# Performance work log

Measured on AMD Instinct MI355X. Metric: run time of the kernel, lower is better.

The kernel has to match this reference:

```python
import jax, jax.numpy as jnp
import numpy as np

B, N = 4, 512
NF, EF = 12, 1          # node / edge feature dims (fixed in GraphClassifier)
QK = 128                # baseFeatNum -> QKDims = nValDims
NV_D, EV_D = 128, 32    # nValDims, eValDims
TR = 2 * NV_D           # Trans output = nValDims*2 = 256
NCLS = 5
EPS = 1e-5


def setup_inputs() -> dict:
    key = jax.random.key(0)
    ks = jax.random.split(key, 16)
    s = 0.1
    return {
        "nodes": jax.random.normal(ks[0], (B, N, NF), jnp.float32),
        "edges": jax.random.normal(ks[1], (B, N, N, EF), jnp.float32),
        "distances": jax.random.uniform(ks[2], (B, N, N), jnp.float32),
        "mask": jax.random.randint(ks[3], (B, N, N), 0, 2) > 0,
        "Wq": jax.random.normal(ks[4], (QK, NF), jnp.float32) * s,
        "bq": jnp.zeros((QK,), jnp.float32),
        "Wk": jax.random.normal(ks[5], (QK, NF), jnp.float32) * s,
        "bk": jnp.zeros((QK,), jnp.float32),
        "Wnv": jax.random.normal(ks[6], (NV_D, NF), jnp.float32) * s,
        "bnv": jnp.zeros((NV_D,), jnp.float32),
        "Wev": jax.random.normal(ks[7], (EV_D, EF), jnp.float32) * s,
        "bev": jnp.zeros((EV_D,), jnp.float32),
        "Wt": jax.random.normal(ks[8], (TR, NV_D + EV_D), jnp.float32) * s,
        "bt": jnp.zeros((TR,), jnp.float32),
        "gamma": jnp.ones((TR,), jnp.float32),
        "beta": jnp.zeros((TR,), jnp.float32),
        "Wc": jax.random.normal(ks[9], (NCLS, TR), jnp.float32) * s,
        "bc": jnp.zeros((NCLS,), jnp.float32),
    }


def reference(nodes, edges, distances, mask, Wq, bq, Wk, bk, Wnv, bnv,
              Wev, bev, Wt, bt, gamma, beta, Wc, bc):
    coeff = 1.0 / np.sqrt(QK).astype(np.float32)
    Q = nodes @ Wq.T + bq            # (b,N,QK)
    K = nodes @ Wk.T + bk            # (b,N,QK)
    NV = nodes @ Wnv.T + bnv         # (b,N,nValDims); NV[b,i,j]=NV_node[b,j] after repeat
    EV = edges @ Wev.T + bev         # (b,N,N,eValDims)

    dist_w = 1.0 / (distances + 1.0)
    scores = jnp.einsum('bik,bjk->bij', Q, K) * dist_w * coeff
    scores = jnp.where(mask, -jnp.inf, scores)
    w = jax.nn.softmax(scores, axis=-1)
    w = jnp.where(jnp.isnan(w), 0.0, w)  # fully-masked rows -> zero weights

    node_part = jnp.einsum('bij,bjd->bid', w, NV)     # weighted node values
    edge_part = jnp.einsum('bij,bijd->bid', w, EV)    # weighted edge values
    vals = jnp.concatenate([node_part, edge_part], axis=-1)
    vals = jnp.tanh(vals) @ Wt.T + bt                 # (b,N,2*nValDims)

    # BatchNorm1d in training mode: biased batch stats over (b*N)
    flat = vals.reshape(-1, TR)
    mu = flat.mean(axis=0)
    var = flat.var(axis=0)
    flat = (flat - mu) / jnp.sqrt(var + EPS) * gamma + beta
    vals = flat.reshape(vals.shape)

    return vals @ Wc.T + bc                           # (b,N,5)
```

## Files before the change

kernel.cpp:

```cpp
#include <hip/hip_runtime.h>
#include <math.h>

#define NNODE 512
#define NBATCH 4
#define NFEAT 12
#define QKD 128
#define NVD 128
#define EVD 32
#define CATD 160
#define CATB 168
#define TRD 256
#define NCLS 5
#define NROWS 2048
#define EPSV 1e-5f
#define NSTATBUF 8
#define NCHUNK 4
#define JC 128
#define RPB 8
#define SSW 132
#define WBW 136

typedef float floatx4 __attribute__((ext_vector_type(4)));
typedef __bf16 bf16x8 __attribute__((ext_vector_type(8)));
typedef unsigned short ushort_t;
typedef ushort_t ushort4v __attribute__((ext_vector_type(4)));

static __device__ __forceinline__ ushort_t f2bf(float x) {
  unsigned int u = __float_as_uint(x);
  return (ushort_t)((u + 0x7fffu + ((u >> 16) & 1u)) >> 16);
}
static __device__ __forceinline__ int slot32(int r) {
  return ((r & 15) >> 2) * 8 + (r & 3) + ((r >> 4) << 2);
}
static __device__ __forceinline__ int kslot(int k) {
  return (k & ~31) + slot32(k & 31);
}

__global__ __launch_bounds__(256) void qkv_kernel(
    const float* __restrict__ nodes,
    const float* __restrict__ Wq, const float* __restrict__ bq,
    const float* __restrict__ Wk, const float* __restrict__ bk,
    const float* __restrict__ Wnv, const float* __restrict__ bnv,
    const float* __restrict__ Wt,
    ushort_t* __restrict__ Qb, ushort_t* __restrict__ Kb,
    ushort_t* __restrict__ NVT, ushort_t* __restrict__ Wtb,
    float* __restrict__ stats) {
  const int tid = threadIdx.x;
  const int blk = blockIdx.x;
  const int rowbase = blk * 8;
  const int b = rowbase >> 9;
  const int jloc = rowbase & (NNODE - 1);
  if (blk < 2 * NSTATBUF) stats[blk * 256 + tid] = 0.f;
  if (tid < CATD)
    Wtb[(size_t)blk * CATD + kslot(tid)] = f2bf(Wt[(size_t)blk * CATD + tid]);
  __shared__ float sn[RPB][NFEAT];
  if (tid < RPB * NFEAT) ((float*)sn)[tid] = nodes[(size_t)rowbase * NFEAT + tid];
  __syncthreads();

  {
    const int d  = tid & 127;
    const int rg = tid >> 7;
    const int sd = kslot(d);
    float wq[NFEAT], wk[NFEAT];
#pragma unroll
    for (int k = 0; k < NFEAT; ++k) {
      wq[k] = Wq[d * NFEAT + k];
      wk[k] = Wk[d * NFEAT + k];
    }
    const float bqv = bq[d], bkv = bk[d];
#pragma unroll
    for (int rr = 0; rr < 4; ++rr) {
      const int rl = rg * 4 + rr;
      float aq = bqv, ak = bkv;
#pragma unroll
      for (int k = 0; k < NFEAT; ++k) {
        const float n = sn[rl][k];
        aq = fmaf(n, wq[k], aq);
        ak = fmaf(n, wk[k], ak);
      }
      Qb[(size_t)(rowbase + rl) * QKD + sd] = f2bf(aq);
      Kb[(size_t)(rowbase + rl) * QKD + sd] = f2bf(ak);
    }
  }
  {
    const int d    = tid >> 1;
    const int half = tid & 1;
    float wnv[NFEAT];
#pragma unroll
    for (int k = 0; k < NFEAT; ++k) wnv[k] = Wnv[d * NFEAT + k];
    const float bnvv = bnv[d];
    ushort4v v;
#pragma unroll
    for (int e = 0; e < 4; ++e) {
      const int rl = half * 4 + e;
      float av = bnvv;
#pragma unroll
      for (int k = 0; k < NFEAT; ++k) av = fmaf(sn[rl][k], wnv[k], av);
      v[e] = f2bf(av);
    }
    const int js = jloc + half * 4;
    const int jsl = (js & ~31) + slot32(js & 31);
    *(ushort4v*)(NVT + (size_t)b * QKD * NNODE + (size_t)d * NNODE + jsl) = v;
  }
}

__global__ __launch_bounds__(512) void attnTrans_kernel(
    const ushort_t* __restrict__ Qb, const ushort_t* __restrict__ Kb,
    const ushort_t* __restrict__ NVT,
    const float* __restrict__ edges, const float* __restrict__ dist,
    const int* __restrict__ mask,
    const float* __restrict__ Wev, const float* __restrict__ bev,
    const ushort_t* __restrict__ Wtb, const float* __restrict__ bt,
    float* __restrict__ vals, float* __restrict__ stats) {
  __shared__ __align__(16) float sS[2][RPB][SSW];
  __shared__ __align__(16) ushort_t sWb[2][16][WBW];
  __shared__ __align__(16) ushort_t catb[RPB * CATB];
  __shared__ float sF[16], sF2[RPB], sSe[RPB], sSw[RPB];

  const int tid = threadIdx.x;
  const int bid = blockIdx.x;
  const int b   = bid >> 6;
  const int rg  = bid & 63;
  const int rowbase = b * NNODE + rg * RPB;

  const int lane = tid & 63;
  const int wv   = tid >> 6;
  const int col  = lane & 15;
  const int kg   = lane >> 4;

  if (tid < 16) sF[tid] = 0.f;

  const int jl  = wv * 16 + col;
  const int dpv = wv * 16 + col;

  bf16x8 aq[4];
  {
    const ushort_t* Qr = Qb + (size_t)(rowbase + (col & 7)) * QKD;
#pragma unroll
    for (int ks = 0; ks < 4; ++ks)
      aq[ks] = *(const bf16x8*)(Qr + ks * 32 + kg * 8);
  }

  bf16x8 kf[2][4], nf[2][4];
  float dd[2][4]; int mm[2][4];
  float ee0[2], ee1[2];
  {
    const ushort_t* Kr = Kb + (size_t)(b * NNODE + jl) * QKD;
    const ushort_t* Nr = NVT + ((size_t)b * QKD + dpv) * NNODE;
#pragma unroll
    for (int ks = 0; ks < 4; ++ks) {
      kf[0][ks] = *(const bf16x8*)(Kr + ks * 32 + kg * 8);
      nf[0][ks] = *(const bf16x8*)(Nr + ks * 32 + kg * 8);
    }
#pragma unroll
    for (int r = 0; r < 4; ++r) {
      const size_t off = (size_t)(rowbase + ((kg * 4 + r) & 7)) * NNODE + jl;
      dd[0][r] = dist[off];
      mm[0][r] = mask[off];
    }
    ee0[0] = edges[(size_t)(rowbase + wv) * NNODE + lane];
    ee1[0] = edges[(size_t)(rowbase + wv) * NNODE + 64 + lane];
  }

  float m_run = -__builtin_inff(), l_run = 0.f, se_run = 0.f;
  floatx4 acc = {0.f, 0.f, 0.f, 0.f};
  const float coeff = 0.0883883476483184f;

#pragma unroll
  for (int c = 0; c < NCHUNK; ++c) {
    const int cur = c & 1, nxt = (c + 1) & 1;
    if (c + 1 < NCHUNK) {
      const int jb2 = (c + 1) * JC;
      const ushort_t* Kr = Kb + (size_t)(b * NNODE + jb2 + jl) * QKD;
      const ushort_t* Nr = NVT + ((size_t)b * QKD + dpv) * NNODE + jb2;
#pragma unroll
      for (int ks = 0; ks < 4; ++ks) {
        kf[nxt][ks] = *(const bf16x8*)(Kr + ks * 32 + kg * 8);
        nf[nxt][ks] = *(const bf16x8*)(Nr + ks * 32 + kg * 8);
      }
#pragma unroll
      for (int r = 0; r < 4; ++r) {
        const size_t off =
            (size_t)(rowbase + ((kg * 4 + r) & 7)) * NNODE + jb2 + jl;
        dd[nxt][r] = dist[off];
        mm[nxt][r] = mask[off];
      }
      ee0[nxt] = edges[(size_t)(rowbase + wv) * NNODE + jb2 + lane];
      ee1[nxt] = edges[(size_t)(rowbase + wv) * NNODE + jb2 + 64 + lane];
    }

    {
      floatx4 sc = {0.f, 0.f, 0.f, 0.f};
#pragma unroll
      for (int ks = 0; ks < 4; ++ks)
        sc = __builtin_amdgcn_mfma_f32_16x16x32_bf16(aq[ks], kf[cur][ks], sc,
                                                     0, 0, 0);
      if (kg < 2) {
#pragma unroll
        for (int r = 0; r < 4; ++r) {
          float s = sc[r] * coeff / (dd[cur][r] + 1.0f);
          if (mm[cur][r]) s = -__builtin_inff();
          sS[cur][kg * 4 + r][jl] = s;
        }
      }
    }
    __syncthreads();

    {
      const float v0 = sS[cur][wv][lane];
      const float v1 = sS[cur][wv][lane + 64];
      float mc = fmaxf(v0, v1);
#pragma unroll
      for (int s = 1; s < 64; s <<= 1) mc = fmaxf(mc, __shfl_xor(mc, s, 64));
      const float mn = fmaxf(m_run, mc);
      const float f = (m_run > -__builtin_inff()) ? __expf(m_run - mn) : 0.f;
      float w0 = 0.f, w1 = 0.f;
      if (mn > -__builtin_inff()) {
        w0 = __expf(v0 - mn);
        w1 = __expf(v1 - mn);
      }
      const int j0 = lane, j1 = lane + 64;
      sWb[cur][wv][(j0 & ~31) + slot32(j0 & 31)] = f2bf(w0);
      sWb[cur][wv][(j1 & ~31) + slot32(j1 & 31)] = f2bf(w1);
      float lc = w0 + w1;
      float sec = fmaf(w0, ee0[cur], w1 * ee1[cur]);
#pragma unroll
      for (int s = 1; s < 64; s <<= 1) {
        lc  += __shfl_xor(lc, s, 64);
        sec += __shfl_xor(sec, s, 64);
      }
      l_run  = l_run * f + lc;
      se_run = se_run * f + sec;
      m_run  = mn;
      if (lane == 0) sF[wv] = f;
    }
    __syncthreads();

    {
      acc[0] *= sF[kg * 4 + 0];
      acc[1] *= sF[kg * 4 + 1];
      acc[2] *= sF[kg * 4 + 2];
      acc[3] *= sF[kg * 4 + 3];
#pragma unroll
      for (int ks = 0; ks < 4; ++ks) {
        const bf16x8 aw =
            *(const bf16x8*)(&sWb[cur][col][ks * 32 + kg * 8]);
        acc = __builtin_amdgcn_mfma_f32_16x16x32_bf16(aw, nf[cur][ks], acc,
                                                      0, 0, 0);
      }
    }
  }

  {
    const float inv = (l_run > 0.f) ? 1.f / l_run : 0.f;
    if (lane == 0) {
      sF2[wv] = inv;
      sSe[wv] = se_run * inv;
      sSw[wv] = (l_run > 0.f) ? 1.f : 0.f;
    }
  }
  __syncthreads();

  if (kg < 2) {
#pragma unroll
    for (int r = 0; r < 4; ++r) {
      const int row = kg * 4 + r;
      catb[row * CATB + kslot(dpv)] = f2bf(tanhf(acc[r] * sF2[row]));
    }
  }
  if (tid < RPB * EVD) {
    const int r = tid >> 5, de = tid & 31;
    catb[r * CATB + 128 + slot32(de)] =
        f2bf(tanhf(fmaf(Wev[de], sSe[r], bev[de] * sSw[r])));
  }
  __syncthreads();

  {
    bf16x8 af[5];
    const ushort_t* cr = catb + (size_t)(col & 7) * CATB;
#pragma unroll
    for (int ks = 0; ks < 5; ++ks)
      af[ks] = *(const bf16x8*)(cr + ks * 32 + kg * 8);
    float* sbuf = stats + (size_t)(bid & (NSTATBUF - 1)) * 2 * TRD;
#pragma unroll
    for (int t = 0; t < 2; ++t) {
      const int o = (wv * 2 + t) * 16 + col;
      const ushort_t* wr = Wtb + (size_t)o * CATD;
      floatx4 a2 = {0.f, 0.f, 0.f, 0.f};
#pragma unroll
      for (int ks = 0; ks < 5; ++ks) {
        const bf16x8 bf = *(const bf16x8*)(wr + ks * 32 + kg * 8);
        a2 = __builtin_amdgcn_mfma_f32_16x16x32_bf16(af[ks], bf, a2, 0, 0, 0);
      }
      const float bto = bt[o];
      float s1 = 0.f, s2 = 0.f;
#pragma unroll
      for (int r = 0; r < 4; ++r) {
        const float v2 = a2[r] + bto;
        if (kg < 2) {
          vals[(size_t)(rowbase + kg * 4 + r) * TRD + o] = v2;
          s1 += v2;
          s2 = fmaf(v2, v2, s2);
        }
      }
      s1 += __shfl_xor(s1, 16, 64); s2 += __shfl_xor(s2, 16, 64);
      s1 += __shfl_xor(s1, 32, 64); s2 += __shfl_xor(s2, 32, 64);
      if (kg == 0) {
        atomicAdd(&sbuf[o], s1);
        atomicAdd(&sbuf[TRD + o], s2);
      }
    }
  }
}

__global__ __launch_bounds__(256) void outbn_kernel(
    const float* __restrict__ vals, const float* __restrict__ stats,
    const float* __restrict__ gamma, const float* __restrict__ beta,
    const float* __restrict__ Wc, const float* __restrict__ bc,
    float* __restrict__ out) {
  __shared__ float sW[NCLS][TRD];
  __shared__ float sb[NCLS];
  __shared__ float red[4][NCLS];
  const int tid = threadIdx.x;
  const int o = tid;
  float s1 = 0.f, s2 = 0.f;
#pragma unroll
  for (int k = 0; k < NSTATBUF; ++k) {
    s1 += stats[k * 2 * TRD + o];
    s2 += stats[k * 2 * TRD + TRD + o];
  }
  const float invN = 1.0f / (float)NROWS;
  const float mu  = s1 * invN;
  const float var = s2 * invN - mu * mu;
  const float inv = 1.0f / sqrtf(var + EPSV);
  const float g = gamma[o] * inv;
  const float bterm = beta[o] - mu * g;
  float v[NCLS];
#pragma unroll
  for (int c = 0; c < NCLS; ++c) {
    const float wc = Wc[c * TRD + o];
    sW[c][o] = wc * g;
    v[c] = wc * bterm;
  }
#pragma unroll
  for (int s = 1; s < 64; s <<= 1) {
#pragma unroll
    for (int c = 0; c < NCLS; ++c) v[c] += __shfl_xor(v[c], s, 64);
  }
  if ((tid & 63) == 0) {
#pragma unroll
    for (int c = 0; c < NCLS; ++c) red[tid >> 6][c] = v[c];
  }
  __syncthreads();
  if (tid < NCLS)
    sb[tid] = bc[tid] + red[0][tid] + red[1][tid] + red[2][tid] + red[3][tid];
  __syncthreads();

  const int lane = tid & 63;
  const int row = blockIdx.x * 4 + (tid >> 6);
  float vv[TRD / 64];
#pragma unroll
  for (int t = 0; t < TRD / 64; ++t)
    vv[t] = vals[(size_t)row * TRD + lane + 64 * t];
#pragma unroll
  for (int c = 0; c < NCLS; ++c) {
    float p = 0.f;
#pragma unroll
    for (int t = 0; t < TRD / 64; ++t)
      p = fmaf(vv[t], sW[c][lane + 64 * t], p);
#pragma unroll
    for (int s = 1; s < 64; s <<= 1) p += __shfl_xor(p, s, 64);
    if (lane == 0) out[(size_t)row * NCLS + c] = p + sb[c];
  }
}

extern "C" void kernel_launch(void* const* d_in, const int* in_sizes, int n_in,
                              void* d_out, int out_size, void* d_ws, size_t ws_size,
                              hipStream_t stream) {
  (void)in_sizes; (void)n_in; (void)out_size; (void)ws_size;
  const float* nodes = (const float*)d_in[0];
  const float* edges = (const float*)d_in[1];
  const float* dist  = (const float*)d_in[2];
  const int*   mask  = (const int*)d_in[3];
  const float* Wq  = (const float*)d_in[4];
  const float* bq  = (const float*)d_in[5];
  const float* Wk  = (const float*)d_in[6];
  const float* bk  = (const float*)d_in[7];
  const float* Wnv = (const float*)d_in[8];
  const float* bnv = (const float*)d_in[9];
  const float* Wev = (const float*)d_in[10];
  const float* bev = (const float*)d_in[11];
  const float* Wt  = (const float*)d_in[12];
  const float* bt  = (const float*)d_in[13];
  const float* gamma = (const float*)d_in[14];
  const float* beta  = (const float*)d_in[15];
  const float* Wc  = (const float*)d_in[16];
  const float* bc  = (const float*)d_in[17];

  char* w = (char*)d_ws;
  ushort_t* Qb  = (ushort_t*)w;                w += (size_t)NROWS * QKD * 2;
  ushort_t* Kb  = (ushort_t*)w;                w += (size_t)NROWS * QKD * 2;
  ushort_t* NVT = (ushort_t*)w;                w += (size_t)NBATCH * QKD * NNODE * 2;
  ushort_t* Wtb = (ushort_t*)w;                w += (size_t)TRD * CATD * 2;
  float* vals  = (float*)w;                    w += (size_t)NROWS * TRD * 4;
  float* stats = (float*)w;
  float* outp  = (float*)d_out;

  qkv_kernel<<<NROWS / RPB, 256, 0, stream>>>(nodes, Wq, bq, Wk, bk, Wnv, bnv,
                                              Wt, Qb, Kb, NVT, Wtb, stats);
  attnTrans_kernel<<<NROWS / RPB, 512, 0, stream>>>(
      Qb, Kb, NVT, edges, dist, mask, Wev, bev, Wtb, bt, vals, stats);
  outbn_kernel<<<NROWS / 4, 256, 0, stream>>>(vals, stats, gamma, beta,
                                              Wc, bc, outp);
}
```

Baseline: 31.91 us.

## Halve rows per attention block, use 4 waves each owning two column tiles

The attention+Trans kernel now handles 4 query rows per block with 256 threads instead of 8 rows with 512, doubling the grid to 512 blocks. Each wave computes two 16-column score and value tiles, and the Trans GEMM loops over four output tiles per wave. This is meant to raise block count and occupancy across CUs and cut per-block sync cost. In exchange, K/NV fragments are loaded by twice as many blocks and 3/4 of MFMA rows are wasted since only 4 of 16 rows are valid.

```diff
diff --git a/kernel.cpp b/kernel.cpp
--- a/kernel.cpp
+++ b/kernel.cpp
@@ -16,7 +16,8 @@
 #define NSTATBUF 8
 #define NCHUNK 4
 #define JC 128
-#define RPB 8
+#define RPB 4
+#define QR 8
 #define SSW 132
 #define WBW 136
 
@@ -47,14 +48,14 @@
     float* __restrict__ stats) {
   const int tid = threadIdx.x;
   const int blk = blockIdx.x;
-  const int rowbase = blk * 8;
+  const int rowbase = blk * QR;
   const int b = rowbase >> 9;
   const int jloc = rowbase & (NNODE - 1);
   if (blk < 2 * NSTATBUF) stats[blk * 256 + tid] = 0.f;
   if (tid < CATD)
     Wtb[(size_t)blk * CATD + kslot(tid)] = f2bf(Wt[(size_t)blk * CATD + tid]);
-  __shared__ float sn[RPB][NFEAT];
-  if (tid < RPB * NFEAT) ((float*)sn)[tid] = nodes[(size_t)rowbase * NFEAT + tid];
+  __shared__ float sn[QR][NFEAT];
+  if (tid < QR * NFEAT) ((float*)sn)[tid] = nodes[(size_t)rowbase * NFEAT + tid];
   __syncthreads();
 
   {
@@ -104,7 +105,7 @@
   }
 }
 
-__global__ __launch_bounds__(512) void attnTrans_kernel(
+__global__ __launch_bounds__(256) void attnTrans_kernel(
     const ushort_t* __restrict__ Qb, const ushort_t* __restrict__ Kb,
     const ushort_t* __restrict__ NVT,
     const float* __restrict__ edges, const float* __restrict__ dist,
@@ -119,8 +120,8 @@
 
   const int tid = threadIdx.x;
   const int bid = blockIdx.x;
-  const int b   = bid >> 6;
-  const int rg  = bid & 63;
+  const int b   = bid >> 7;
+  const int rg  = bid & 127;
   const int rowbase = b * NNODE + rg * RPB;
 
   const int lane = tid & 63;
@@ -130,40 +131,56 @@
 
   if (tid < 16) sF[tid] = 0.f;
 
-  const int jl  = wv * 16 + col;
-  const int dpv = wv * 16 + col;
+  const int jl0 = (wv * 2) * 16 + col;
+  const int jl1 = jl0 + 16;
+  const int dp0 = (wv * 2) * 16 + col;
+  const int dp1 = dp0 + 16;
 
   bf16x8 aq[4];
   {
-    const ushort_t* Qr = Qb + (size_t)(rowbase + (col & 7)) * QKD;
+    const ushort_t* Qr = Qb + (size_t)(rowbase + (col & 3)) * QKD;
 #pragma unroll
     for (int ks = 0; ks < 4; ++ks)
       aq[ks] = *(const bf16x8*)(Qr + ks * 32 + kg * 8);
   }
 
-  bf16x8 kf[2][4], nf[2][4];
-  float dd[2][4]; int mm[2][4];
+  bf16x8 kf[2][2][4], nf[2][2][4];
+  float dd0[2][4], dd1[2][4];
+  int   mm0[2][4], mm1[2][4];
   float ee0[2], ee1[2];
   {
-    const ushort_t* Kr = Kb + (size_t)(b * NNODE + jl) * QKD;
-    const ushort_t* Nr = NVT + ((size_t)b * QKD + dpv) * NNODE;
+    const ushort_t* K0 = Kb + (size_t)(b * NNODE + jl0) * QKD;
+    const ushort_t* K1 = Kb + (size_t)(b * NNODE + jl1) * QKD;
+    const ushort_t* N0 = NVT + ((size_t)b * QKD + dp0) * NNODE;
+    const ushort_t* N1 = NVT + ((size_t)b * QKD + dp1) * NNODE;
 #pragma unroll
     for (int ks = 0; ks < 4; ++ks) {
-      kf[0][ks] = *(const bf16x8*)(Kr + ks * 32 + kg * 8);
-      nf[0][ks] = *(const bf16x8*)(Nr + ks * 32 + kg * 8);
-    }
-#pragma unroll
-    for (int r = 0; r < 4; ++r) {
-      const size_t off = (size_t)(rowbase + ((kg * 4 + r) & 7)) * NNODE + jl;
-      dd[0][r] = dist[off];
-      mm[0][r] = mask[off];
+      kf[0][0][ks] = *(const bf16x8*)(K0 + ks * 32 + kg * 8);
+      kf[0][1][ks] = *(const bf16x8*)(K1 + ks * 32 + kg * 8);
+      nf[0][0][ks] = *(const bf16x8*)(N0 + ks * 32 + kg * 8);
+      nf[0][1][ks] = *(const bf16x8*)(N1 + ks * 32 + kg * 8);
+    }
+    if (kg == 0) {
+#pragma unroll
+      for (int r = 0; r < 4; ++r) {
+        const size_t off = (size_t)(rowbase + r) * NNODE;
+        dd0[0][r] = dist[off + jl0]; mm0[0][r] = mask[off + jl0];
+        dd1[0][r] = dist[off + jl1]; mm1[0][r] = mask[off + jl1];
+      }
+    } else {
+#pragma unroll
+      for (int r = 0; r < 4; ++r) {
+        dd0[0][r] = 0.f; mm0[0][r] = 0;
+        dd1[0][r] = 0.f; mm1[0][r] = 0;
+      }
     }
     ee0[0] = edges[(size_t)(rowbase + wv) * NNODE + lane];
     ee1[0] = edges[(size_t)(rowbase + wv) * NNODE + 64 + lane];
   }
 
   float m_run = -__builtin_inff(), l_run = 0.f, se_run = 0.f;
-  floatx4 acc = {0.f, 0.f, 0.f, 0.f};
+  floatx4 acc0 = {0.f, 0.f, 0.f, 0.f};
+  floatx4 acc1 = {0.f, 0.f, 0.f, 0.f};
   const float coeff = 0.0883883476483184f;
 
 #pragma unroll
@@ -171,36 +188,54 @@
     const int cur = c & 1, nxt = (c + 1) & 1;
     if (c + 1 < NCHUNK) {
       const int jb2 = (c + 1) * JC;
-      const ushort_t* Kr = Kb + (size_t)(b * NNODE + jb2 + jl) * QKD;
-      const ushort_t* Nr = NVT + ((size_t)b * QKD + dpv) * NNODE + jb2;
+      const ushort_t* K0 = Kb + (size_t)(b * NNODE + jb2 + jl0) * QKD;
+      const ushort_t* K1 = Kb + (size_t)(b * NNODE + jb2 + jl1) * QKD;
+      const ushort_t* N0 = NVT + ((size_t)b * QKD + dp0) * NNODE + jb2;
+      const ushort_t* N1 = NVT + ((size_t)b * QKD + dp1) * NNODE + jb2;
 #pragma unroll
       for (int ks = 0; ks < 4; ++ks) {
-        kf[nxt][ks] = *(const bf16x8*)(Kr + ks * 32 + kg * 8);
-        nf[nxt][ks] = *(const bf16x8*)(Nr + ks * 32 + kg * 8);
-      }
-#pragma unroll
-      for (int r = 0; r < 4; ++r) {
-        const size_t off =
-            (size_t)(rowbase + ((kg * 4 + r) & 7)) * NNODE + jb2 + jl;
-        dd[nxt][r] = dist[off];
-        mm[nxt][r] = mask[off];
+        kf[nxt][0][ks] = *(const bf16x8*)(K0 + ks * 32 + kg * 8);
+        kf[nxt][1][ks] = *(const bf16x8*)(K1 + ks * 32 + kg * 8);
+        nf[nxt][0][ks] = *(const bf16x8*)(N0 + ks * 32 + kg * 8);
+        nf[nxt][1][ks] = *(const bf16x8*)(N1 + ks * 32 + kg * 8);
+      }
+      if (kg == 0) {
+#pragma unroll
+        for (int r = 0; r < 4; ++r) {
+          const size_t off = (size_t)(rowbase + r) * NNODE + jb2;
+          dd0[nxt][r] = dist[off + jl0]; mm0[nxt][r] = mask[off + jl0];
+          dd1[nxt][r] = dist[off + jl1]; mm1[nxt][r] = mask[off + jl1];
+        }
+      } else {
+#pragma unroll
+        for (int r = 0; r < 4; ++r) {
+          dd0[nxt][r] = 0.f; mm0[nxt][r] = 0;
+          dd1[nxt][r] = 0.f; mm1[nxt][r] = 0;
+        }
       }
       ee0[nxt] = edges[(size_t)(rowbase + wv) * NNODE + jb2 + lane];
       ee1[nxt] = edges[(size_t)(rowbase + wv) * NNODE + jb2 + 64 + lane];
     }
 
     {
-      floatx4 sc = {0.f, 0.f, 0.f, 0.f};
-#pragma unroll
-      for (int ks = 0; ks < 4; ++ks)
-        sc = __builtin_amdgcn_mfma_f32_16x16x32_bf16(aq[ks], kf[cur][ks], sc,
-                                                     0, 0, 0);
-      if (kg < 2) {
+      floatx4 sc0 = {0.f, 0.f, 0.f, 0.f};
+      floatx4 sc1 = {0.f, 0.f, 0.f, 0.f};
+#pragma unroll
+      for (int ks = 0; ks < 4; ++ks) {
+        sc0 = __builtin_amdgcn_mfma_f32_16x16x32_bf16(aq[ks], kf[cur][0][ks],
+                                                      sc0, 0, 0, 0);
+        sc1 = __builtin_amdgcn_mfma_f32_16x16x32_bf16(aq[ks], kf[cur][1][ks],
+                                                      sc1, 0, 0, 0);
+      }
+      if (kg == 0) {
 #pragma unroll
         for (int r = 0; r < 4; ++r) {
-          float s = sc[r] * coeff / (dd[cur][r] + 1.0f);
-          if (mm[cur][r]) s = -__builtin_inff();
-          sS[cur][kg * 4 + r][jl] = s;
+          float s0 = sc0[r] * coeff / (dd0[cur][r] + 1.0f);
+          if (mm0[cur][r]) s0 = -__builtin_inff();
+          sS[cur][r][jl0] = s0;
+          float s1 = sc1[r] * coeff / (dd1[cur][r] + 1.0f);
+          if (mm1[cur][r]) s1 = -__builtin_inff();
+          sS[cur][r][jl1] = s1;
         }
       }
     }
@@ -237,16 +272,18 @@
     __syncthreads();
 
     {
-      acc[0] *= sF[kg * 4 + 0];
-      acc[1] *= sF[kg * 4 + 1];
-      acc[2] *= sF[kg * 4 + 2];
-      acc[3] *= sF[kg * 4 + 3];
+      const float f0 = sF[kg * 4 + 0], f1 = sF[kg * 4 + 1];
+      const float f2 = sF[kg * 4 + 2], f3 = sF[kg * 4 + 3];
+      acc0[0] *= f0; acc0[1] *= f1; acc0[2] *= f2; acc0[3] *= f3;
+      acc1[0] *= f0; acc1[1] *= f1; acc1[2] *= f2; acc1[3] *= f3;
 #pragma unroll
       for (int ks = 0; ks < 4; ++ks) {
         const bf16x8 aw =
             *(const bf16x8*)(&sWb[cur][col][ks * 32 + kg * 8]);
-        acc = __builtin_amdgcn_mfma_f32_16x16x32_bf16(aw, nf[cur][ks], acc,
-                                                      0, 0, 0);
+        acc0 = __builtin_amdgcn_mfma_f32_16x16x32_bf16(aw, nf[cur][0][ks],
+                                                       acc0, 0, 0, 0);
+        acc1 = __builtin_amdgcn_mfma_f32_16x16x32_bf16(aw, nf[cur][1][ks],
+                                                       acc1, 0, 0, 0);
       }
     }
   }
@@ -261,11 +298,11 @@
   }
   __syncthreads();
 
-  if (kg < 2) {
+  if (kg == 0) {
 #pragma unroll
     for (int r = 0; r < 4; ++r) {
-      const int row = kg * 4 + r;
-      catb[row * CATB + kslot(dpv)] = f2bf(tanhf(acc[r] * sF2[row]));
+      catb[r * CATB + kslot(dp0)] = f2bf(tanhf(acc0[r] * sF2[r]));
+      catb[r * CATB + kslot(dp1)] = f2bf(tanhf(acc1[r] * sF2[r]));
     }
   }
   if (tid < RPB * EVD) {
@@ -277,14 +314,14 @@
 
   {
     bf16x8 af[5];
-    const ushort_t* cr = catb + (size_t)(col & 7) * CATB;
+    const ushort_t* cr = catb + (size_t)(col & 3) * CATB;
 #pragma unroll
     for (int ks = 0; ks < 5; ++ks)
       af[ks] = *(const bf16x8*)(cr + ks * 32 + kg * 8);
     float* sbuf = stats + (size_t)(bid & (NSTATBUF - 1)) * 2 * TRD;
 #pragma unroll
-    for (int t = 0; t < 2; ++t) {
-      const int o = (wv * 2 + t) * 16 + col;
+    for (int t = 0; t < 4; ++t) {
+      const int o = (wv * 4 + t) * 16 + col;
       const ushort_t* wr = Wtb + (size_t)o * CATD;
       floatx4 a2 = {0.f, 0.f, 0.f, 0.f};
 #pragma unroll
@@ -297,8 +334,8 @@
 #pragma unroll
       for (int r = 0; r < 4; ++r) {
         const float v2 = a2[r] + bto;
-        if (kg < 2) {
-          vals[(size_t)(rowbase + kg * 4 + r) * TRD + o] = v2;
+        if (kg == 0) {
+          vals[(size_t)(rowbase + r) * TRD + o] = v2;
           s1 += v2;
           s2 = fmaf(v2, v2, s2);
         }
@@ -406,9 +443,9 @@
   float* stats = (float*)w;
   float* outp  = (float*)d_out;
 
-  qkv_kernel<<<NROWS / RPB, 256, 0, stream>>>(nodes, Wq, bq, Wk, bk, Wnv, bnv,
-                                              Wt, Qb, Kb, NVT, Wtb, stats);
-  attnTrans_kernel<<<NROWS / RPB, 512, 0, stream>>>(
+  qkv_kernel<<<NROWS / QR, 256, 0, stream>>>(nodes, Wq, bq, Wk, bk, Wnv, bnv,
+                                             Wt, Qb, Kb, NVT, Wtb, stats);
+  attnTrans_kernel<<<NROWS / RPB, 256, 0, stream>>>(
       Qb, Kb, NVT, edges, dist, mask, Wev, bev, Wtb, bt, vals, stats);
   outbn_kernel<<<NROWS / 4, 256, 0, stream>>>(vals, stats, gamma, beta,
                                               Wc, bc, outp);
```

After: 42.47 us. 33.1% more time.

## Process attention keys in two 256-wide chunks with manual prefetch

Applied to the files above, without the earlier changes.

The online-softmax loop over four 128-key chunks is replaced by two explicit 256-key chunks. Each wave now computes two score tiles and runs eight PV MFMAs per chunk, and the second chunk's K, NV, dist, mask and edge loads are issued before the first chunk's softmax. This halves the number of block barriers and softmax rescale steps. The cost is more live registers, which may lower occupancy or cause spills. The qkv kernel only gets a constant renamed.

```diff
diff --git a/kernel.cpp b/kernel.cpp
--- a/kernel.cpp
+++ b/kernel.cpp
@@ -14,11 +14,11 @@
 #define NROWS 2048
 #define EPSV 1e-5f
 #define NSTATBUF 8
-#define NCHUNK 4
-#define JC 128
+#define JC2 256
 #define RPB 8
-#define SSW 132
-#define WBW 136
+#define QR 8
+#define SSW2 264
+#define WBW2 272
 
 typedef float floatx4 __attribute__((ext_vector_type(4)));
 typedef __bf16 bf16x8 __attribute__((ext_vector_type(8)));
@@ -47,14 +47,14 @@
     float* __restrict__ stats) {
   const int tid = threadIdx.x;
   const int blk = blockIdx.x;
-  const int rowbase = blk * 8;
+  const int rowbase = blk * QR;
   const int b = rowbase >> 9;
   const int jloc = rowbase & (NNODE - 1);
   if (blk < 2 * NSTATBUF) stats[blk * 256 + tid] = 0.f;
   if (tid < CATD)
     Wtb[(size_t)blk * CATD + kslot(tid)] = f2bf(Wt[(size_t)blk * CATD + tid]);
-  __shared__ float sn[RPB][NFEAT];
-  if (tid < RPB * NFEAT) ((float*)sn)[tid] = nodes[(size_t)rowbase * NFEAT + tid];
+  __shared__ float sn[QR][NFEAT];
+  if (tid < QR * NFEAT) ((float*)sn)[tid] = nodes[(size_t)rowbase * NFEAT + tid];
   __syncthreads();
 
   {
@@ -112,8 +112,8 @@
     const float* __restrict__ Wev, const float* __restrict__ bev,
     const ushort_t* __restrict__ Wtb, const float* __restrict__ bt,
     float* __restrict__ vals, float* __restrict__ stats) {
-  __shared__ __align__(16) float sS[2][RPB][SSW];
-  __shared__ __align__(16) ushort_t sWb[2][16][WBW];
+  __shared__ __align__(16) float sS[RPB][SSW2];
+  __shared__ __align__(16) ushort_t sWb[16][WBW2];
   __shared__ __align__(16) ushort_t catb[RPB * CATB];
   __shared__ float sF[16], sF2[RPB], sSe[RPB], sSw[RPB];
 
@@ -130,7 +130,8 @@
 
   if (tid < 16) sF[tid] = 0.f;
 
-  const int jl  = wv * 16 + col;
+  const int jt0 = wv * 32 + col;
+  const int jt1 = jt0 + 16;
   const int dpv = wv * 16 + col;
 
   bf16x8 aq[4];
@@ -141,113 +142,183 @@
       aq[ks] = *(const bf16x8*)(Qr + ks * 32 + kg * 8);
   }
 
-  bf16x8 kf[2][4], nf[2][4];
-  float dd[2][4]; int mm[2][4];
-  float ee0[2], ee1[2];
-  {
-    const ushort_t* Kr = Kb + (size_t)(b * NNODE + jl) * QKD;
+  bf16x8 k0a[4], k0b[4], n0[8];
+  float dd0a[4], dd0b[4]; int mm0a[4], mm0b[4]; float e0[4];
+  {
+    const ushort_t* K0 = Kb + (size_t)(b * NNODE + jt0) * QKD;
+    const ushort_t* K1 = Kb + (size_t)(b * NNODE + jt1) * QKD;
     const ushort_t* Nr = NVT + ((size_t)b * QKD + dpv) * NNODE;
 #pragma unroll
     for (int ks = 0; ks < 4; ++ks) {
-      kf[0][ks] = *(const bf16x8*)(Kr + ks * 32 + kg * 8);
-      nf[0][ks] = *(const bf16x8*)(Nr + ks * 32 + kg * 8);
-    }
+      k0a[ks] = *(const bf16x8*)(K0 + ks * 32 + kg * 8);
+      k0b[ks] = *(const bf16x8*)(K1 + ks * 32 + kg * 8);
+    }
+#pragma unroll
+    for (int ks = 0; ks < 8; ++ks)
+      n0[ks] = *(const bf16x8*)(Nr + ks * 32 + kg * 8);
 #pragma unroll
     for (int r = 0; r < 4; ++r) {
-      const size_t off = (size_t)(rowbase + ((kg * 4 + r) & 7)) * NNODE + jl;
-      dd[0][r] = dist[off];
-      mm[0][r] = mask[off];
-    }
-    ee0[0] = edges[(size_t)(rowbase + wv) * NNODE + lane];
-    ee1[0] = edges[(size_t)(rowbase + wv) * NNODE + 64 + lane];
+      const size_t off = (size_t)(rowbase + ((kg * 4 + r) & 7)) * NNODE;
+      dd0a[r] = dist[off + jt0]; mm0a[r] = mask[off + jt0];
+      dd0b[r] = dist[off + jt1]; mm0b[r] = mask[off + jt1];
+    }
+#pragma unroll
+    for (int t = 0; t < 4; ++t)
+      e0[t] = edges[(size_t)(rowbase + wv) * NNODE + lane + 64 * t];
   }
 
   float m_run = -__builtin_inff(), l_run = 0.f, se_run = 0.f;
   floatx4 acc = {0.f, 0.f, 0.f, 0.f};
   const float coeff = 0.0883883476483184f;
 
-#pragma unroll
-  for (int c = 0; c < NCHUNK; ++c) {
-    const int cur = c & 1, nxt = (c + 1) & 1;
-    if (c + 1 < NCHUNK) {
-      const int jb2 = (c + 1) * JC;
-      const ushort_t* Kr = Kb + (size_t)(b * NNODE + jb2 + jl) * QKD;
-      const ushort_t* Nr = NVT + ((size_t)b * QKD + dpv) * NNODE + jb2;
-#pragma unroll
-      for (int ks = 0; ks < 4; ++ks) {
-        kf[nxt][ks] = *(const bf16x8*)(Kr + ks * 32 + kg * 8);
-        nf[nxt][ks] = *(const bf16x8*)(Nr + ks * 32 + kg * 8);
-      }
+  {
+    floatx4 sc0 = {0.f, 0.f, 0.f, 0.f};
+    floatx4 sc1 = {0.f, 0.f, 0.f, 0.f};
+#pragma unroll
+    for (int ks = 0; ks < 4; ++ks) {
+      sc0 = __builtin_amdgcn_mfma_f32_16x16x32_bf16(aq[ks], k0a[ks], sc0, 0, 0, 0);
+      sc1 = __builtin_amdgcn_mfma_f32_16x16x32_bf16(aq[ks], k0b[ks], sc1, 0, 0, 0);
+    }
+    if (kg < 2) {
 #pragma unroll
       for (int r = 0; r < 4; ++r) {
-        const size_t off =
-            (size_t)(rowbase + ((kg * 4 + r) & 7)) * NNODE + jb2 + jl;
-        dd[nxt][r] = dist[off];
-        mm[nxt][r] = mask[off];
-      }
-      ee0[nxt] = edges[(size_t)(rowbase + wv) * NNODE + jb2 + lane];
-      ee1[nxt] = edges[(size_t)(rowbase + wv) * NNODE + jb2 + 64 + lane];
-    }
-
-    {
-      floatx4 sc = {0.f, 0.f, 0.f, 0.f};
-#pragma unroll
-      for (int ks = 0; ks < 4; ++ks)
-        sc = __builtin_amdgcn_mfma_f32_16x16x32_bf16(aq[ks], kf[cur][ks], sc,
-                                                     0, 0, 0);
-      if (kg < 2) {
-#pragma unroll
-        for (int r = 0; r < 4; ++r) {
-          float s = sc[r] * coeff / (dd[cur][r] + 1.0f);
-          if (mm[cur][r]) s = -__builtin_inff();
-          sS[cur][kg * 4 + r][jl] = s;
-        }
-      }
-    }
-    __syncthreads();
-
-    {
-      const float v0 = sS[cur][wv][lane];
-      const float v1 = sS[cur][wv][lane + 64];
-      float mc = fmaxf(v0, v1);
-#pragma unroll
-      for (int s = 1; s < 64; s <<= 1) mc = fmaxf(mc, __shfl_xor(mc, s, 64));
-      const float mn = fmaxf(m_run, mc);
-      const float f = (m_run > -__builtin_inff()) ? __expf(m_run - mn) : 0.f;
-      float w0 = 0.f, w1 = 0.f;
-      if (mn > -__builtin_inff()) {
-        w0 = __expf(v0 - mn);
-        w1 = __expf(v1 - mn);
-      }
-      const int j0 = lane, j1 = lane + 64;
-      sWb[cur][wv][(j0 & ~31) + slot32(j0 & 31)] = f2bf(w0);
-      sWb[cur][wv][(j1 & ~31) + slot32(j1 & 31)] = f2bf(w1);
-      float lc = w0 + w1;
-      float sec = fmaf(w0, ee0[cur], w1 * ee1[cur]);
-#pragma unroll
-      for (int s = 1; s < 64; s <<= 1) {
-        lc  += __shfl_xor(lc, s, 64);
-        sec += __shfl_xor(sec, s, 64);
-      }
-      l_run  = l_run * f + lc;
-      se_run = se_run * f + sec;
-      m_run  = mn;
-      if (lane == 0) sF[wv] = f;
-    }
-    __syncthreads();
-
-    {
-      acc[0] *= sF[kg * 4 + 0];
-      acc[1] *= sF[kg * 4 + 1];
-      acc[2] *= sF[kg * 4 + 2];
-      acc[3] *= sF[kg * 4 + 3];
-#pragma unroll
-      for (int ks = 0; ks < 4; ++ks) {
-        const bf16x8 aw =
-            *(const bf16x8*)(&sWb[cur][col][ks * 32 + kg * 8]);
-        acc = __builtin_amdgcn_mfma_f32_16x16x32_bf16(aw, nf[cur][ks], acc,
-                                                      0, 0, 0);
-      }
+        float s0 = sc0[r] * coeff / (dd0a[r] + 1.0f);
+        if (mm0a[r]) s0 = -__builtin_inff();
+        sS[kg * 4 + r][jt0] = s0;
+        float s1 = sc1[r] * coeff / (dd0b[r] + 1.0f);
+        if (mm0b[r]) s1 = -__builtin_inff();
+        sS[kg * 4 + r][jt1] = s1;
+      }
+    }
+  }
+  bf16x8 k1a[4], k1b[4], n1[8];
+  float dd1a[4], dd1b[4]; int mm1a[4], mm1b[4]; float e1[4];
+  {
+    const ushort_t* K0 = Kb + (size_t)(b * NNODE + JC2 + jt0) * QKD;
+    const ushort_t* K1 = Kb + (size_t)(b * NNODE + JC2 + jt1) * QKD;
+    const ushort_t* Nr = NVT + ((size_t)b * QKD + dpv) * NNODE + JC2;
+#pragma unroll
+    for (int ks = 0; ks < 4; ++ks) {
+      k1a[ks] = *(const bf16x8*)(K0 + ks * 32 + kg * 8);
+      k1b[ks] = *(const bf16x8*)(K1 + ks * 32 + kg * 8);
+    }
+#pragma unroll
+    for (int ks = 0; ks < 8; ++ks)
+      n1[ks] = *(const bf16x8*)(Nr + ks * 32 + kg * 8);
+#pragma unroll
+    for (int r = 0; r < 4; ++r) {
+      const size_t off = (size_t)(rowbase + ((kg * 4 + r) & 7)) * NNODE + JC2;
+      dd1a[r] = dist[off + jt0]; mm1a[r] = mask[off + jt0];
+      dd1b[r] = dist[off + jt1]; mm1b[r] = mask[off + jt1];
+    }
+#pragma unroll
+    for (int t = 0; t < 4; ++t)
+      e1[t] = edges[(size_t)(rowbase + wv) * NNODE + JC2 + lane + 64 * t];
+  }
+  __syncthreads();
+
+  {
+    float v[4];
+#pragma unroll
+    for (int t = 0; t < 4; ++t) v[t] = sS[wv][lane + 64 * t];
+    float mc = fmaxf(fmaxf(v[0], v[1]), fmaxf(v[2], v[3]));
+#pragma unroll
+    for (int s = 1; s < 64; s <<= 1) mc = fmaxf(mc, __shfl_xor(mc, s, 64));
+    const float mn = fmaxf(m_run, mc);
+    const float f = (m_run > -__builtin_inff()) ? __expf(m_run - mn) : 0.f;
+    float w[4], lc = 0.f, sec = 0.f;
+#pragma unroll
+    for (int t = 0; t < 4; ++t) {
+      w[t] = (mn > -__builtin_inff()) ? __expf(v[t] - mn) : 0.f;
+      const int j = lane + 64 * t;
+      sWb[wv][(j & ~31) + slot32(j & 31)] = f2bf(w[t]);
+      lc += w[t];
+      sec = fmaf(w[t], e0[t], sec);
+    }
+#pragma unroll
+    for (int s = 1; s < 64; s <<= 1) {
+      lc  += __shfl_xor(lc, s, 64);
+      sec += __shfl_xor(sec, s, 64);
+    }
+    l_run  = l_run * f + lc;
+    se_run = se_run * f + sec;
+    m_run  = mn;
+    if (lane == 0) sF[wv] = f;
+  }
+  __syncthreads();
+
+  {
+    acc[0] *= sF[kg * 4 + 0];
+    acc[1] *= sF[kg * 4 + 1];
+    acc[2] *= sF[kg * 4 + 2];
+    acc[3] *= sF[kg * 4 + 3];
+#pragma unroll
+    for (int ks = 0; ks < 8; ++ks) {
+      const bf16x8 aw = *(const bf16x8*)(&sWb[col][ks * 32 + kg * 8]);
+      acc = __builtin_amdgcn_mfma_f32_16x16x32_bf16(aw, n0[ks], acc, 0, 0, 0);
+    }
+  }
+
+  {
+    floatx4 sc0 = {0.f, 0.f, 0.f, 0.f};
+    floatx4 sc1 = {0.f, 0.f, 0.f, 0.f};
+#pragma unroll
+    for (int ks = 0; ks < 4; ++ks) {
+      sc0 = __builtin_amdgcn_mfma_f32_16x16x32_bf16(aq[ks], k1a[ks], sc0, 0, 0, 0);
+      sc1 = __builtin_amdgcn_mfma_f32_16x16x32_bf16(aq[ks], k1b[ks], sc1, 0, 0, 0);
+    }
+    if (kg < 2) {
+#pragma unroll
+      for (int r = 0; r < 4; ++r) {
+        float s0 = sc0[r] * coeff / (dd1a[r] + 1.0f);
+        if (mm1a[r]) s0 = -__builtin_inff();
+        sS[kg * 4 + r][jt0] = s0;
+        float s1 = sc1[r] * coeff / (dd1b[r] + 1.0f);
+        if (mm1b[r]) s1 = -__builtin_inff();
+        sS[kg * 4 + r][jt1] = s1;
+      }
+    }
+  }
+  __syncthreads();
+  {
+    float v[4];
+#pragma unroll
+    for (int t = 0; t < 4; ++t) v[t] = sS[wv][lane + 64 * t];
+    float mc = fmaxf(fmaxf(v[0], v[1]), fmaxf(v[2], v[3]));
+#pragma unroll
+    for (int s = 1; s < 64; s <<= 1) mc = fmaxf(mc, __shfl_xor(mc, s, 64));
+    const float mn = fmaxf(m_run, mc);
+    const float f = (m_run > -__builtin_inff()) ? __expf(m_run - mn) : 0.f;
+    float w[4], lc = 0.f, sec = 0.f;
+#pragma unroll
+    for (int t = 0; t < 4; ++t) {
+      w[t] = (mn > -__builtin_inff()) ? __expf(v[t] - mn) : 0.f;
+      const int j = lane + 64 * t;
+      sWb[wv][(j & ~31) + slot32(j & 31)] = f2bf(w[t]);
+      lc += w[t];
+      sec = fmaf(w[t], e1[t], sec);
+    }
+#pragma unroll
+    for (int s = 1; s < 64; s <<= 1) {
+      lc  += __shfl_xor(lc, s, 64);
+      sec += __shfl_xor(sec, s, 64);
+    }
+    l_run  = l_run * f + lc;
+    se_run = se_run * f + sec;
+    m_run  = mn;
+    if (lane == 0) sF[wv] = f;
+  }
+  __syncthreads();
+
+  {
+    acc[0] *= sF[kg * 4 + 0];
+    acc[1] *= sF[kg * 4 + 1];
+    acc[2] *= sF[kg * 4 + 2];
+    acc[3] *= sF[kg * 4 + 3];
+#pragma unroll
+    for (int ks = 0; ks < 8; ++ks) {
+      const bf16x8 aw = *(const bf16x8*)(&sWb[col][ks * 32 + kg * 8]);
+      acc = __builtin_amdgcn_mfma_f32_16x16x32_bf16(aw, n1[ks], acc, 0, 0, 0);
     }
   }
 
@@ -406,8 +477,8 @@
   float* stats = (float*)w;
   float* outp  = (float*)d_out;
 
-  qkv_kernel<<<NROWS / RPB, 256, 0, stream>>>(nodes, Wq, bq, Wk, bk, Wnv, bnv,
-                                              Wt, Qb, Kb, NVT, Wtb, stats);
+  qkv_kernel<<<NROWS / QR, 256, 0, stream>>>(nodes, Wq, bq, Wk, bk, Wnv, bnv,
+                                             Wt, Qb, Kb, NVT, Wtb, stats);
   attnTrans_kernel<<<NROWS / RPB, 512, 0, stream>>>(
       Qb, Kb, NVT, edges, dist, mask, Wev, bev, Wtb, bt, vals, stats);
   outbn_kernel<<<NROWS / 4, 256, 0, stream>>>(vals, stats, gamma, beta,
```

Result: faster. 31.14 us (-2.4%).
